# Kernel tuning notes

Measured on AMD Instinct MI355X. Metric: run time of the kernel, lower is better.

The kernel has to match this reference:

```python
import jax, jax.numpy as jnp
import numpy as np

BN, L, DM = 2, 1024, 1024
D_STATE, D_CONV, EXPAND = 16, 4, 2
D_INNER = DM * EXPAND


def setup_inputs() -> dict:
    key = jax.random.key(0)
    ks = jax.random.split(key, 12)
    s = lambda fan: 1.0 / np.sqrt(fan)
    x = jax.random.normal(ks[0], (BN, L, DM), jnp.float32)
    in_w = jax.random.normal(ks[1], (DM, 2 * D_INNER), jnp.float32) * s(DM)
    in_b = jnp.zeros((2 * D_INNER,), jnp.float32)
    # depthwise conv kernel, flax layout (window, in_per_group=1, features)
    conv_w = jax.random.normal(ks[2], (D_CONV, 1, D_INNER), jnp.float32) * s(D_CONV)
    conv_b = jnp.zeros((D_INNER,), jnp.float32)
    # negative A for a stable scan (exp(dt*A) <= 1), as in real Mamba
    A = -jax.random.uniform(ks[3], (D_INNER, D_STATE), jnp.float32, 0.1, 1.0)
    Dp = jnp.ones((D_INNER,), jnp.float32)
    B_w = jax.random.normal(ks[4], (D_INNER, D_STATE), jnp.float32) * s(D_INNER)
    B_b = jnp.zeros((D_STATE,), jnp.float32)
    C_w = jax.random.normal(ks[5], (D_INNER, D_STATE), jnp.float32) * s(D_INNER)
    C_b = jnp.zeros((D_STATE,), jnp.float32)
    dt_w = jax.random.normal(ks[6], (D_INNER, D_INNER), jnp.float32) * s(D_INNER)
    dt_b = jnp.full((D_INNER,), -4.0, jnp.float32)  # softplus -> small dt
    out_w = jax.random.normal(ks[7], (D_INNER, DM), jnp.float32) * s(D_INNER)
    out_b = jnp.zeros((DM,), jnp.float32)
    return {"x": x, "in_w": in_w, "in_b": in_b, "conv_w": conv_w, "conv_b": conv_b,
            "A": A, "Dp": Dp, "B_w": B_w, "B_b": B_b, "C_w": C_w, "C_b": C_b,
            "dt_w": dt_w, "dt_b": dt_b, "out_w": out_w, "out_b": out_b}


def reference(x, in_w, in_b, conv_w, conv_b, A, Dp, B_w, B_b, C_w, C_b, dt_w, dt_b, out_w, out_b):
    Bn, Ln, _ = x.shape
    d_inner, d_state = A.shape
    xp = x @ in_w + in_b                      # [B,L,2*d_inner]
    x_z, gate = jnp.split(xp, 2, axis=-1)
    # depthwise causal-ish SAME conv along L
    x_conv = jax.lax.conv_general_dilated(
        x_z, conv_w, window_strides=(1,), padding='SAME',
        dimension_numbers=('NWC', 'WIO', 'NWC'), feature_group_count=d_inner) + conv_b
    x_conv = jax.nn.silu(x_conv)              # [B,L,d_inner]
    Bm = x_conv @ B_w + B_b                   # [B,L,d_state]
    Cm = x_conv @ C_w + C_b                   # [B,L,d_state]
    dt = jax.nn.softplus(x_conv @ dt_w + dt_b)  # [B,L,d_inner]
    dA = jnp.exp(dt[..., None] * A[None, None])     # [B,L,d_inner,d_state]
    dB = dt[..., None] * Bm[..., None, :]           # [B,L,d_inner,d_state]

    def scan_fn(h, inp):
        x_t, dA_t, dB_t, C_t = inp            # [B,d_inner], [B,d_inner,S]x2, [B,S]
        h = dA_t * h + dB_t * x_t[..., None]
        y_t = jnp.sum(h * C_t[:, None, :], axis=-1)  # [B,d_inner]
        return h, y_t

    h0 = jnp.zeros((Bn, d_inner, d_state), x.dtype)
    tm = lambda t: jnp.swapaxes(t, 0, 1)      # time-major
    _, y = jax.lax.scan(scan_fn, h0, (tm(x_conv), tm(dA), tm(dB), tm(Cm)))
    y = jnp.swapaxes(y, 0, 1)                 # [B,L,d_inner]
    y = y + x_conv * Dp
    y = y * jax.nn.silu(gate)
    return y @ out_w + out_b                  # [B,L,d_model]
```

## Files before the change

kernel.cpp:

```cpp
#include <hip/hip_runtime.h>
#include <hip/hip_bf16.h>
#include <math.h>

#define BN_   2
#define L_    1024
#define DM_   1024
#define DS_   16
#define DI_   2048
#define M_    (BN_ * L_)
#define NBC_  2176

typedef __attribute__((ext_vector_type(8))) short short8;
typedef __attribute__((ext_vector_type(4))) float f32x4;

__device__ __forceinline__ unsigned short f2b(float f) {
    union { float f; unsigned u; } x; x.f = f;
    unsigned r = x.u + 0x7fffu + ((x.u >> 16) & 1u);
    return (unsigned short)(r >> 16);
}
__device__ __forceinline__ float b2f(unsigned short u) {
    union { unsigned u; float f; } x; x.u = ((unsigned)u) << 16; return x.f;
}

__device__ __forceinline__ void gload_lds16(const unsigned short* g, unsigned short* l) {
    __builtin_amdgcn_global_load_lds(
        (const __attribute__((address_space(1))) void*)g,
        (__attribute__((address_space(3))) void*)l, 16, 0, 0);
}

__device__ __forceinline__ void tr_tile(
    const float* __restrict__ in, unsigned short* __restrict__ out,
    int R, int C, int bx, int by)
{
    __shared__ float t[32][33];
    const int tx = threadIdx.x & 31;
    const int ty = (threadIdx.x >> 5) * 4;
    #pragma unroll
    for (int j = 0; j < 4; ++j)
        t[ty + j][tx] = in[(size_t)(by + ty + j) * C + bx + tx];
    __syncthreads();
    #pragma unroll
    for (int j = 0; j < 4; ++j)
        out[(size_t)(bx + ty + j) * R + by + tx] = f2b(t[tx][ty + j]);
}

__global__ __launch_bounds__(256) void prep(
    const float* __restrict__ x,
    const float* __restrict__ in_w, const float* __restrict__ dt_w,
    const float* __restrict__ out_w,
    const float* __restrict__ Bw, const float* __restrict__ Cw,
    unsigned short* __restrict__ xb, unsigned short* __restrict__ w1,
    unsigned short* __restrict__ w2, unsigned short* __restrict__ w3)
{
    const int blk = blockIdx.x;
    const int tid = threadIdx.x;
    if (blk < 2048) {
        const int i = (blk * 256 + tid) * 4;
        if (i < M_ * DM_) {
            float4 v = *(const float4*)(x + i);
            ushort4 o; o.x = f2b(v.x); o.y = f2b(v.y); o.z = f2b(v.z); o.w = f2b(v.w);
            *(ushort4*)(xb + i) = o;
        }
    } else if (blk < 6144) {
        const int id = blk - 2048;
        tr_tile(in_w, w1, DM_, 2 * DI_, (id & 127) * 32, (id >> 7) * 32);
    } else if (blk < 10240) {
        const int id = blk - 6144;
        tr_tile(dt_w, w2, DI_, DI_, (id & 63) * 32, (id >> 6) * 32);
    } else if (blk < 12288) {
        const int id = blk - 10240;
        tr_tile(out_w, w3, DI_, DM_, (id & 31) * 32, (id >> 5) * 32);
    } else {
        const int idx = (blk - 12288) * 256 + tid;
        const int r = idx >> 11;
        const int k = idx & 2047;
        const float* src = (r < 16) ? Bw : Cw;
        w2[(size_t)(2048 + r) * 2048 + k] = f2b(src[k * 16 + (r & 15)]);
    }
}

template<int BM, int BN, int MODE>
__global__ __launch_bounds__(512) void gemm_mfma(
    const unsigned short* __restrict__ A,
    const unsigned short* __restrict__ Bt,
    const float* __restrict__ b0, const float* __restrict__ b1,
    const float* __restrict__ b2,
    float* __restrict__ F0, float* __restrict__ F1, float* __restrict__ F2,
    unsigned short* __restrict__ U0, unsigned short* __restrict__ U1,
    int M, int N, int K, int NS)
{
    constexpr int MF  = BM / 32;
    constexpr int NF  = BN / 64;
    constexpr int ACW = BM / 64;
    constexpr int BCW = BN / 64;

    __shared__ unsigned short Asl[2][BM * 64];
    __shared__ unsigned short Bsl[2][BN * 64];

    const int tid  = threadIdx.x;
    const int wave = tid >> 6;
    const int lane = tid & 63;

    const int gx  = gridDim.x, gy = gridDim.y;
    const int bid = blockIdx.y * gx + blockIdx.x;
    const int q   = (gx * gy) >> 3;
    const int nb  = (bid & 7) * q + (bid >> 3);
    const int by  = nb % gy;
    const int bx  = nb / gy;

    const int row0 = by * BM;
    const int col0 = bx * BN;
    const int wr   = (wave >> 2) * (BM / 2);
    const int wc   = (wave & 3) * (BN / 4);

    const int srow = lane >> 3;
    const int scol = ((lane & 7) ^ (lane >> 3)) * 8;

    auto stage = [&](int buf, int kt) {
        #pragma unroll
        for (int i = 0; i < ACW; ++i) {
            const int ch = wave * ACW + i;
            gload_lds16(A + (size_t)(row0 + ch * 8 + srow) * K + kt + scol,
                        &Asl[buf][ch * 512]);
        }
        #pragma unroll
        for (int i = 0; i < BCW; ++i) {
            const int ch = wave * BCW + i;
            gload_lds16(Bt + (size_t)(col0 + ch * 8 + srow) * K + kt + scol,
                        &Bsl[buf][ch * 512]);
        }
    };

    f32x4 acc[MF][NF];
    #pragma unroll
    for (int m = 0; m < MF; ++m)
        #pragma unroll
        for (int n = 0; n < NF; ++n)
            acc[m][n] = (f32x4){0.f, 0.f, 0.f, 0.f};

    stage(0, 0);
    __syncthreads();

    const int nk = K >> 6;
    int cur = 0;
    for (int kt = 0; kt < nk; ++kt) {
        if (kt + 1 < nk) stage(cur ^ 1, (kt + 1) << 6);

        short8 af[MF][2], bf[NF][2];
        const int lrow  = lane & 15;
        const int xsw   = (lane & 7) * 8;
        const int cbase = (lane >> 4) * 8;
        #pragma unroll
        for (int m = 0; m < MF; ++m)
            #pragma unroll
            for (int kk = 0; kk < 2; ++kk)
                af[m][kk] = *(const short8*)
                    &Asl[cur][(wr + m * 16 + lrow) * 64 + ((kk * 32 + cbase) ^ xsw)];
        #pragma unroll
        for (int n = 0; n < NF; ++n)
            #pragma unroll
            for (int kk = 0; kk < 2; ++kk)
                bf[n][kk] = *(const short8*)
                    &Bsl[cur][(wc + n * 16 + lrow) * 64 + ((kk * 32 + cbase) ^ xsw)];

        #pragma unroll
        for (int m = 0; m < MF; ++m)
            #pragma unroll
            for (int n = 0; n < NF; ++n) {
                acc[m][n] = __builtin_amdgcn_mfma_f32_16x16x32_bf16(
                    af[m][0], bf[n][0], acc[m][n], 0, 0, 0);
                acc[m][n] = __builtin_amdgcn_mfma_f32_16x16x32_bf16(
                    af[m][1], bf[n][1], acc[m][n], 0, 0, 0);
            }
        __syncthreads();
        cur ^= 1;
    }

    const int crow = (lane >> 4) * 4;
    const int ccol = lane & 15;
    #pragma unroll
    for (int m = 0; m < MF; ++m)
        #pragma unroll
        for (int n = 0; n < NF; ++n) {
            const int c = col0 + wc + n * 16 + ccol;
            if (MODE == 0) {
                const float bv = b0[c];
                unsigned short* dst = (c < NS) ? (U0 + c) : (U1 + (c - NS));
                #pragma unroll
                for (int j = 0; j < 4; ++j) {
                    const int r = row0 + wr + m * 16 + crow + j;
                    dst[(size_t)r * NS] = f2b(acc[m][n][j] + bv);
                }
            } else if (MODE == 1) {
                if (c < 2048) {
                    const float bv = b0[c];
                    #pragma unroll
                    for (int j = 0; j < 4; ++j) {
                        const int r = row0 + wr + m * 16 + crow + j;
                        float v = acc[m][n][j] + bv;
                        v = (v > 20.0f) ? v : log1pf(__expf(v));
                        U0[(size_t)r * 2048 + c] = f2b(v);
                    }
                } else if (c < 2064) {
                    const float bv = b1[c - 2048];
                    #pragma unroll
                    for (int j = 0; j < 4; ++j) {
                        const int r = row0 + wr + m * 16 + crow + j;
                        F1[(size_t)r * 16 + (c - 2048)] = acc[m][n][j] + bv;
                    }
                } else if (c < 2080) {
                    const float bv = b2[c - 2064];
                    #pragma unroll
                    for (int j = 0; j < 4; ++j) {
                        const int r = row0 + wr + m * 16 + crow + j;
                        F2[(size_t)r * 16 + (c - 2064)] = acc[m][n][j] + bv;
                    }
                }
            } else {
                const float bv = b0[c];
                #pragma unroll
                for (int j = 0; j < 4; ++j) {
                    const int r = row0 + wr + m * 16 + crow + j;
                    F0[(size_t)r * NS + c] = acc[m][n][j] + bv;
                }
            }
        }
}

__global__ __launch_bounds__(256) void conv_silu(
    const unsigned short* __restrict__ xzb, const float* __restrict__ cw,
    const float* __restrict__ cb, unsigned short* __restrict__ xcb)
{
    const int idx = blockIdx.x * 256 + threadIdx.x;
    if (idx >= BN_ * L_ * DI_) return;
    const int d = idx & (DI_ - 1);
    const int t = (idx / DI_) & (L_ - 1);
    const int b = idx / (DI_ * L_);

    float acc = cb[d];
    #pragma unroll
    for (int w = 0; w < 4; ++w) {
        const int tt = t + w - 1;
        if (tt >= 0 && tt < L_)
            acc = fmaf(b2f(xzb[((size_t)(b * L_ + tt)) * DI_ + d]), cw[w * DI_ + d], acc);
    }
    const float s = acc / (1.0f + __expf(-acc));
    xcb[idx] = f2b(s);
}

#define NCH_ 32
#define TL_  (L_ / NCH_)

__global__ __launch_bounds__(256) void scan_part1(
    const unsigned short* __restrict__ dt, const unsigned short* __restrict__ xcb,
    const float* __restrict__ Bm, const float* __restrict__ A,
    float* __restrict__ Pc, float* __restrict__ Hc)
{
    const int tid = threadIdx.x;
    const int d   = blockIdx.x * 256 + tid;
    const int b   = blockIdx.y;
    const int j   = blockIdx.z;
    const int t0  = j * TL_;

    __shared__ float s_Bm[TL_ * DS_];
    {
        const float* src = Bm + ((size_t)b * L_ + t0) * DS_;
        s_Bm[tid]       = src[tid];
        s_Bm[256 + tid] = src[256 + tid];
    }
    float a[DS_];
    #pragma unroll
    for (int qq = 0; qq < 4; ++qq)
        *(float4*)&a[qq * 4] = *(const float4*)(A + (size_t)d * DS_ + qq * 4);
    __syncthreads();

    const unsigned short* dtp = dt + ((size_t)b * L_ + t0) * DI_ + d;
    const unsigned short* xcp = xcb + ((size_t)b * L_ + t0) * DI_ + d;

    float h[DS_] = {};
    float P[DS_];
    #pragma unroll
    for (int s = 0; s < DS_; ++s) P[s] = 1.0f;

    float dtv = b2f(dtp[0]), xcv = b2f(xcp[0]);
    #pragma unroll 4
    for (int t = 0; t < TL_; ++t) {
        float dtv_n = 0.f, xcv_n = 0.f;
        if (t + 1 < TL_) {
            dtv_n = b2f(dtp[(size_t)(t + 1) * DI_]);
            xcv_n = b2f(xcp[(size_t)(t + 1) * DI_]);
        }
        const float dx = dtv * xcv;
        #pragma unroll
        for (int qq = 0; qq < 4; ++qq) {
            const float4 bm = *(const float4*)&s_Bm[t * DS_ + qq * 4];
            #pragma unroll
            for (int i = 0; i < 4; ++i) {
                const int s = qq * 4 + i;
                const float bv = (i == 0) ? bm.x : (i == 1) ? bm.y : (i == 2) ? bm.z : bm.w;
                const float dA = __expf(dtv * a[s]);
                P[s] *= dA;
                h[s] = fmaf(dA, h[s], dx * bv);
            }
        }
        dtv = dtv_n; xcv = xcv_n;
    }
    const size_t o0 = (((size_t)b * NCH_ + j) * DS_) * DI_ + d;
    #pragma unroll
    for (int s = 0; s < DS_; ++s) {
        Pc[o0 + (size_t)s * DI_] = P[s];
        Hc[o0 + (size_t)s * DI_] = h[s];
    }
}

__global__ __launch_bounds__(256) void scan_combine(
    const float* __restrict__ Pc, float* __restrict__ Hc)
{
    const size_t idx = (size_t)blockIdx.x * 256 + threadIdx.x;
    const size_t b   = idx / (DS_ * DI_);
    const size_t rem = idx % (DS_ * DI_);
    const size_t base   = b * ((size_t)NCH_ * DS_ * DI_) + rem;
    const size_t stride = (size_t)DS_ * DI_;
    float h = 0.f;
    #pragma unroll
    for (int j = 0; j < NCH_; ++j) {
        const size_t o = base + (size_t)j * stride;
        const float P  = Pc[o];
        const float hl = Hc[o];
        Hc[o] = h;
        h = fmaf(P, h, hl);
    }
}

__global__ __launch_bounds__(256) void scan_part2(
    const unsigned short* __restrict__ dt, const unsigned short* __restrict__ xcb,
    const unsigned short* __restrict__ gate,
    const float* __restrict__ Bm, const float* __restrict__ Cm,
    const float* __restrict__ A, const float* __restrict__ Dp,
    const float* __restrict__ Hin, unsigned short* __restrict__ ygb)
{
    const int tid = threadIdx.x;
    const int d   = blockIdx.x * 256 + tid;
    const int b   = blockIdx.y;
    const int j   = blockIdx.z;
    const int t0  = j * TL_;

    __shared__ float s_Bm[TL_ * DS_];
    __shared__ float s_Cm[TL_ * DS_];
    {
        const float* bsrc = Bm + ((size_t)b * L_ + t0) * DS_;
        const float* csrc = Cm + ((size_t)b * L_ + t0) * DS_;
        s_Bm[tid]       = bsrc[tid];
        s_Bm[256 + tid] = bsrc[256 + tid];
        s_Cm[tid]       = csrc[tid];
        s_Cm[256 + tid] = csrc[256 + tid];
    }
    float a[DS_];
    #pragma unroll
    for (int qq = 0; qq < 4; ++qq)
        *(float4*)&a[qq * 4] = *(const float4*)(A + (size_t)d * DS_ + qq * 4);
    const float dp = Dp[d];

    float h[DS_];
    {
        const size_t o0 = (((size_t)b * NCH_ + j) * DS_) * DI_ + d;
        #pragma unroll
        for (int s = 0; s < DS_; ++s) h[s] = Hin[o0 + (size_t)s * DI_];
    }
    __syncthreads();

    const size_t rbase = ((size_t)b * L_ + t0) * DI_ + d;
    const unsigned short* dtp = dt   + rbase;
    const unsigned short* xcp = xcb  + rbase;
    const unsigned short* gvp = gate + rbase;
    unsigned short* yp = ygb + rbase;

    float dtv = b2f(dtp[0]), xcv = b2f(xcp[0]), gv = b2f(gvp[0]);
    #pragma unroll 4
    for (int t = 0; t < TL_; ++t) {
        float dtv_n = 0.f, xcv_n = 0.f, gv_n = 0.f;
        if (t + 1 < TL_) {
            dtv_n = b2f(dtp[(size_t)(t + 1) * DI_]);
            xcv_n = b2f(xcp[(size_t)(t + 1) * DI_]);
            gv_n  = b2f(gvp[(size_t)(t + 1) * DI_]);
        }
        const float dx = dtv * xcv;
        float y0 = 0.f, y1 = 0.f, y2 = 0.f, y3 = 0.f;
        #pragma unroll
        for (int qq = 0; qq < 4; ++qq) {
            const float4 bm = *(const float4*)&s_Bm[t * DS_ + qq * 4];
            const float4 cm = *(const float4*)&s_Cm[t * DS_ + qq * 4];
            #pragma unroll
            for (int i = 0; i < 4; ++i) {
                const int s = qq * 4 + i;
                const float bv = (i == 0) ? bm.x : (i == 1) ? bm.y : (i == 2) ? bm.z : bm.w;
                const float cv = (i == 0) ? cm.x : (i == 1) ? cm.y : (i == 2) ? cm.z : cm.w;
                const float dA = __expf(dtv * a[s]);
                h[s] = fmaf(dA, h[s], dx * bv);
                if (i == 0) y0 = fmaf(h[s], cv, y0);
                else if (i == 1) y1 = fmaf(h[s], cv, y1);
                else if (i == 2) y2 = fmaf(h[s], cv, y2);
                else y3 = fmaf(h[s], cv, y3);
            }
        }
        float y = (y0 + y1) + (y2 + y3);
        y = fmaf(xcv, dp, y);
        const float r = y * (gv / (1.0f + __expf(-gv)));
        yp[(size_t)t * DI_] = f2b(r);
        dtv = dtv_n; xcv = xcv_n; gv = gv_n;
    }
}

extern "C" void kernel_launch(void* const* d_in, const int* in_sizes, int n_in,
                              void* d_out, int out_size, void* d_ws, size_t ws_size,
                              hipStream_t stream)
{
    const float* x      = (const float*)d_in[0];
    const float* in_w   = (const float*)d_in[1];
    const float* in_b   = (const float*)d_in[2];
    const float* conv_w = (const float*)d_in[3];
    const float* conv_b = (const float*)d_in[4];
    const float* A      = (const float*)d_in[5];
    const float* Dp     = (const float*)d_in[6];
    const float* B_w    = (const float*)d_in[7];
    const float* B_b    = (const float*)d_in[8];
    const float* C_w    = (const float*)d_in[9];
    const float* C_b    = (const float*)d_in[10];
    const float* dt_w   = (const float*)d_in[11];
    const float* dt_b   = (const float*)d_in[12];
    const float* out_w  = (const float*)d_in[13];
    const float* out_b  = (const float*)d_in[14];
    float* out = (float*)d_out;

    unsigned short* dtb = (unsigned short*)d_ws;
    float* Bm   = (float*)(dtb + (size_t)M_ * DI_);
    float* Cm   = Bm  + (size_t)M_ * DS_;
    unsigned short* w3  = (unsigned short*)(Cm + (size_t)M_ * DS_);
    unsigned short* w1  = w3  + (size_t)DM_ * DI_;
    unsigned short* xb  = w1  + (size_t)2 * DI_ * DM_;
    unsigned short* w2  = xb  + (size_t)M_ * DM_;
    unsigned short* xcb = w2  + (size_t)NBC_ * DI_;
    unsigned short* xzb = xcb + (size_t)M_ * DI_;
    unsigned short* gtb = xzb + (size_t)M_ * DI_;
    unsigned short* ygb = xcb;
    float* Pc = (float*)w1;
    float* Hc = (float*)xb;

    prep<<<12544, 256, 0, stream>>>(x, in_w, dt_w, out_w, B_w, C_w, xb, w1, w2, w3);

    gemm_mfma<64, 128, 0><<<dim3(2 * DI_ / 128, M_ / 64), 512, 0, stream>>>(
        xb, w1, in_b, nullptr, nullptr,
        nullptr, nullptr, nullptr, xzb, gtb, M_, 2 * DI_, DM_, DI_);

    conv_silu<<<(BN_ * L_ * DI_) / 256, 256, 0, stream>>>(xzb, conv_w, conv_b, xcb);

    gemm_mfma<64, 128, 1><<<dim3(NBC_ / 128, M_ / 64), 512, 0, stream>>>(
        xcb, w2, dt_b, B_b, C_b,
        nullptr, Bm, Cm, dtb, nullptr, M_, NBC_, DI_, NBC_);

    scan_part1<<<dim3(DI_ / 256, BN_, NCH_), 256, 0, stream>>>(
        dtb, xcb, Bm, A, Pc, Hc);
    scan_combine<<<(BN_ * DI_ * DS_) / 256, 256, 0, stream>>>(Pc, Hc);
    scan_part2<<<dim3(DI_ / 256, BN_, NCH_), 256, 0, stream>>>(
        dtb, xcb, gtb, Bm, Cm, A, Dp, Hc, ygb);

    gemm_mfma<64, 64, 2><<<dim3(DM_ / 64, M_ / 64), 512, 0, stream>>>(
        ygb, w3, out_b, nullptr, nullptr,
        out, nullptr, nullptr, nullptr, nullptr, M_, DM_, DI_, DM_);
}
```

Baseline: 169.2 us.

## Vectorize conv_silu, double scan chunks, store chunk carries in bf16

The depthwise conv+SiLU kernel now has each thread handle 8 channels with 128-bit bf16 loads and stores instead of one scalar element. The scan is split into 64 chunks of 16 steps instead of 32 chunks of 32, which gives more blocks and shorter serial loops per thread. The per-chunk decay products and carry states are stored as bf16 instead of fp32, halving that intermediate traffic even though twice as many chunk records now exist. Rounding the carries to bf16 adds error to the recurrence, and the combine pass becomes twice as long serially.

```diff
diff --git a/kernel.cpp b/kernel.cpp
--- a/kernel.cpp
+++ b/kernel.cpp
@@ -232,29 +232,42 @@
     const float* __restrict__ cb, unsigned short* __restrict__ xcb)
 {
     const int idx = blockIdx.x * 256 + threadIdx.x;
-    if (idx >= BN_ * L_ * DI_) return;
-    const int d = idx & (DI_ - 1);
-    const int t = (idx / DI_) & (L_ - 1);
-    const int b = idx / (DI_ * L_);
-
-    float acc = cb[d];
+    const int nd8 = DI_ / 8;
+    const int d0  = (idx & (nd8 - 1)) * 8;
+    const int r   = idx / nd8;
+    const int t   = r & (L_ - 1);
+    const int b   = r >> 10;
+
+    float acc[8];
+    #pragma unroll
+    for (int j = 0; j < 8; ++j) acc[j] = cb[d0 + j];
+
     #pragma unroll
     for (int w = 0; w < 4; ++w) {
         const int tt = t + w - 1;
-        if (tt >= 0 && tt < L_)
-            acc = fmaf(b2f(xzb[((size_t)(b * L_ + tt)) * DI_ + d]), cw[w * DI_ + d], acc);
-    }
-    const float s = acc / (1.0f + __expf(-acc));
-    xcb[idx] = f2b(s);
-}
-
-#define NCH_ 32
+        if (tt >= 0 && tt < L_) {
+            const short8 v = *(const short8*)(xzb + ((size_t)(b * L_ + tt)) * DI_ + d0);
+            #pragma unroll
+            for (int j = 0; j < 8; ++j)
+                acc[j] = fmaf(b2f((unsigned short)v[j]), cw[w * DI_ + d0 + j], acc[j]);
+        }
+    }
+    short8 o;
+    #pragma unroll
+    for (int j = 0; j < 8; ++j) {
+        const float s = acc[j] / (1.0f + __expf(-acc[j]));
+        o[j] = (short)f2b(s);
+    }
+    *(short8*)(xcb + (size_t)r * DI_ + d0) = o;
+}
+
+#define NCH_ 64
 #define TL_  (L_ / NCH_)
 
 __global__ __launch_bounds__(256) void scan_part1(
     const unsigned short* __restrict__ dt, const unsigned short* __restrict__ xcb,
     const float* __restrict__ Bm, const float* __restrict__ A,
-    float* __restrict__ Pc, float* __restrict__ Hc)
+    unsigned short* __restrict__ Pc, unsigned short* __restrict__ Hc)
 {
     const int tid = threadIdx.x;
     const int d   = blockIdx.x * 256 + tid;
@@ -265,8 +278,7 @@
     __shared__ float s_Bm[TL_ * DS_];
     {
         const float* src = Bm + ((size_t)b * L_ + t0) * DS_;
-        s_Bm[tid]       = src[tid];
-        s_Bm[256 + tid] = src[256 + tid];
+        s_Bm[tid] = src[tid];
     }
     float a[DS_];
     #pragma unroll
@@ -308,13 +320,13 @@
     const size_t o0 = (((size_t)b * NCH_ + j) * DS_) * DI_ + d;
     #pragma unroll
     for (int s = 0; s < DS_; ++s) {
-        Pc[o0 + (size_t)s * DI_] = P[s];
-        Hc[o0 + (size_t)s * DI_] = h[s];
+        Pc[o0 + (size_t)s * DI_] = f2b(P[s]);
+        Hc[o0 + (size_t)s * DI_] = f2b(h[s]);
     }
 }
 
 __global__ __launch_bounds__(256) void scan_combine(
-    const float* __restrict__ Pc, float* __restrict__ Hc)
+    const unsigned short* __restrict__ Pc, unsigned short* __restrict__ Hc)
 {
     const size_t idx = (size_t)blockIdx.x * 256 + threadIdx.x;
     const size_t b   = idx / (DS_ * DI_);
@@ -322,12 +334,12 @@
     const size_t base   = b * ((size_t)NCH_ * DS_ * DI_) + rem;
     const size_t stride = (size_t)DS_ * DI_;
     float h = 0.f;
-    #pragma unroll
+    #pragma unroll 8
     for (int j = 0; j < NCH_; ++j) {
         const size_t o = base + (size_t)j * stride;
-        const float P  = Pc[o];
-        const float hl = Hc[o];
-        Hc[o] = h;
+        const float P  = b2f(Pc[o]);
+        const float hl = b2f(Hc[o]);
+        Hc[o] = f2b(h);
         h = fmaf(P, h, hl);
     }
 }
@@ -337,7 +349,7 @@
     const unsigned short* __restrict__ gate,
     const float* __restrict__ Bm, const float* __restrict__ Cm,
     const float* __restrict__ A, const float* __restrict__ Dp,
-    const float* __restrict__ Hin, unsigned short* __restrict__ ygb)
+    const unsigned short* __restrict__ Hin, unsigned short* __restrict__ ygb)
 {
     const int tid = threadIdx.x;
     const int d   = blockIdx.x * 256 + tid;
@@ -350,10 +362,8 @@
     {
         const float* bsrc = Bm + ((size_t)b * L_ + t0) * DS_;
         const float* csrc = Cm + ((size_t)b * L_ + t0) * DS_;
-        s_Bm[tid]       = bsrc[tid];
-        s_Bm[256 + tid] = bsrc[256 + tid];
-        s_Cm[tid]       = csrc[tid];
-        s_Cm[256 + tid] = csrc[256 + tid];
+        s_Bm[tid] = bsrc[tid];
+        s_Cm[tid] = csrc[tid];
     }
     float a[DS_];
     #pragma unroll
@@ -365,7 +375,7 @@
     {
         const size_t o0 = (((size_t)b * NCH_ + j) * DS_) * DI_ + d;
         #pragma unroll
-        for (int s = 0; s < DS_; ++s) h[s] = Hin[o0 + (size_t)s * DI_];
+        for (int s = 0; s < DS_; ++s) h[s] = b2f(Hin[o0 + (size_t)s * DI_]);
     }
     __syncthreads();
 
@@ -443,8 +453,8 @@
     unsigned short* xzb = xcb + (size_t)M_ * DI_;
     unsigned short* gtb = xzb + (size_t)M_ * DI_;
     unsigned short* ygb = xcb;
-    float* Pc = (float*)w1;
-    float* Hc = (float*)xb;
+    unsigned short* Pc = w1;
+    unsigned short* Hc = xb;
 
     prep<<<12544, 256, 0, stream>>>(x, in_w, dt_w, out_w, B_w, C_w, xb, w1, w2, w3);
 
@@ -452,7 +462,7 @@
         xb, w1, in_b, nullptr, nullptr,
         nullptr, nullptr, nullptr, xzb, gtb, M_, 2 * DI_, DM_, DI_);
 
-    conv_silu<<<(BN_ * L_ * DI_) / 256, 256, 0, stream>>>(xzb, conv_w, conv_b, xcb);
+    conv_silu<<<(BN_ * L_ * DI_ / 8) / 256, 256, 0, stream>>>(xzb, conv_w, conv_b, xcb);
 
     gemm_mfma<64, 128, 1><<<dim3(NBC_ / 128, M_ / 64), 512, 0, stream>>>(
         xcb, w2, dt_b, B_b, C_b,
```

Result: faster. 165.5 us (median of 2 runs) (-2.2%).
